# Kernel tuning notes

Hardware: AMD Instinct MI355X
Metric: run time of the kernel (lower is better)

Reference implementation:

```python
import jax, jax.numpy as jnp
import numpy as np

NS = 10000   # servers
ND = 50000   # devices
H = 512      # hidden dim
E = 300000   # edges per relation
L = 4        # total SAGEConv layers (input + 2 hidden + output)


def segment_mean(vals, seg, num_segments):
    # scatter-mean aggregation (PyG 'mean' aggr); empty segments -> 0
    s = jax.ops.segment_sum(vals, seg, num_segments=num_segments)
    cnt = jax.ops.segment_sum(jnp.ones((seg.shape[0], 1), vals.dtype), seg,
                              num_segments=num_segments)
    return s / jnp.maximum(cnt, 1.0)


def setup_inputs() -> dict:
    key = jax.random.key(0)
    ks = jax.random.split(key, 12)
    scale = 0.05
    return {
        "x_servers": jax.random.normal(ks[0], (NS, 64), jnp.float32),
        "x_devices": jax.random.normal(ks[1], (ND, 32), jnp.float32),
        "W_srv": jax.random.normal(ks[2], (64, H), jnp.float32) * scale,
        "b_srv": jnp.zeros((H,), jnp.float32),
        "W_dev": jax.random.normal(ks[3], (32, H), jnp.float32) * scale,
        "b_dev": jnp.zeros((H,), jnp.float32),
        # rel 0: servers->devices (updates devices); rel 1: devices->servers
        "Wl": jax.random.normal(ks[4], (L, 2, H, H), jnp.float32) * scale,
        "bl": jnp.zeros((L, 2, H), jnp.float32),
        "Wr": jax.random.normal(ks[5], (L, 2, H, H), jnp.float32) * scale,
        "e_sd_src": jax.random.randint(ks[6], (E,), 0, NS, jnp.int32),
        "e_sd_dst": jax.random.randint(ks[7], (E,), 0, ND, jnp.int32),
        "e_ds_src": jax.random.randint(ks[8], (E,), 0, ND, jnp.int32),
        "e_ds_dst": jax.random.randint(ks[9], (E,), 0, NS, jnp.int32),
    }


def reference(x_servers, x_devices, W_srv, b_srv, W_dev, b_dev,
              Wl, bl, Wr, e_sd_src, e_sd_dst, e_ds_src, e_ds_dst):
    # per-type input projection (no activation, as in GNN.forward)
    hs = x_servers @ W_srv + b_srv   # [NS, H]
    hd = x_devices @ W_dev + b_dev   # [ND, H]
    for l in range(L):
        # gather source features per edge, scatter-mean to destination
        agg_d = segment_mean(hs[e_sd_src], e_sd_dst, ND)  # servers -> devices
        agg_s = segment_mean(hd[e_ds_src], e_ds_dst, NS)  # devices -> servers
        # SAGEConv: lin_l(agg) + lin_r(x_dst), then relu
        new_d = jax.nn.relu(agg_d @ Wl[l, 0] + bl[l, 0] + hd @ Wr[l, 0])
        new_s = jax.nn.relu(agg_s @ Wl[l, 1] + bl[l, 1] + hs @ Wr[l, 1])
        hs, hd = new_s, new_d
    return (hs, hd)
```

## Files before the change

### kernel.cpp

```cpp
#include <hip/hip_runtime.h>
#include <cstdint>

#define NSRV 10000
#define NDEV 50000
#define HDIM 512
#define NEDGE 300000
#define NLAY 4
#define SCHUNK 2048

typedef unsigned int u32;
typedef unsigned short u16;

typedef __bf16 bf16x8 __attribute__((ext_vector_type(8)));
typedef float f32x4 __attribute__((ext_vector_type(4)));

__device__ __forceinline__ float bflo(u32 u) { return __uint_as_float(u << 16); }
__device__ __forceinline__ float bfhi(u32 u) { return __uint_as_float(u & 0xffff0000u); }
__device__ __forceinline__ float bf2f(u16 v) { return __uint_as_float((u32)v << 16); }
__device__ __forceinline__ u16 f2bf(float f) {
    u32 u = __float_as_uint(f);
    u += 0x7fffu + ((u >> 16) & 1u);
    return (u16)(u >> 16);
}
__device__ __forceinline__ u32 pack2(float a, float b) {
    return (u32)f2bf(a) | ((u32)f2bf(b) << 16);
}

__global__ void cast_bf16(const float* __restrict__ src, u16* __restrict__ dst, int n2) {
    int i = blockIdx.x * 256 + threadIdx.x;
    if (i < n2) {
        float2 v = *(const float2*)(src + 2 * (size_t)i);
        *(u32*)(dst + 2 * (size_t)i) = pack2(v.x, v.y);
    }
}

__global__ void transpose_w(const float* __restrict__ Wl, const float* __restrict__ Wr,
                            u16* __restrict__ WlT, u16* __restrict__ WrT) {
    __shared__ float t[32][33];
    int z = blockIdx.z;
    const float* Wsrc = ((z < 8) ? Wl : Wr) + (size_t)(z & 7) * HDIM * HDIM;
    u16* Wdst = ((z < 8) ? WlT : WrT) + (size_t)(z & 7) * HDIM * HDIM;
    int n0 = blockIdx.x * 32, k0 = blockIdx.y * 32;
    int x = threadIdx.x, y = threadIdx.y;
#pragma unroll
    for (int i = 0; i < 4; ++i)
        t[y + 8 * i][x] = Wsrc[(size_t)(k0 + y + 8 * i) * HDIM + n0 + x];
    __syncthreads();
    if (x < 16) {
#pragma unroll
        for (int i = 0; i < 4; ++i) {
            int n = n0 + y + 8 * i;
            u32 v = pack2(t[2 * x][y + 8 * i], t[2 * x + 1][y + 8 * i]);
            *(u32*)(Wdst + (size_t)n * HDIM + k0 + 2 * x) = v;
        }
    }
}

template <int K>
__global__ void transpose_wp(const float* __restrict__ W, u16* __restrict__ WT) {
    __shared__ float t[32][33];
    int n0 = blockIdx.x * 32, k0 = blockIdx.y * 32;
    int x = threadIdx.x, y = threadIdx.y;
#pragma unroll
    for (int i = 0; i < 4; ++i)
        t[y + 8 * i][x] = W[(size_t)(k0 + y + 8 * i) * HDIM + n0 + x];
    __syncthreads();
    if (x < 16) {
#pragma unroll
        for (int i = 0; i < 4; ++i) {
            int n = n0 + y + 8 * i;
            u32 v = pack2(t[2 * x][y + 8 * i], t[2 * x + 1][y + 8 * i]);
            *(u32*)(WT + (size_t)n * K + k0 + 2 * x) = v;
        }
    }
}

template <int KTOT>
__launch_bounds__(256, 2)
__global__ void proj_gemm(const u16* __restrict__ A, const u16* __restrict__ B,
                          const float* __restrict__ bias, u16* __restrict__ C, int M) {
    constexpr int NKC = KTOT / 8;
    __shared__ __align__(16) u16 As[NKC][128][8];
    __shared__ __align__(16) u16 Bs[NKC][128][8];
    const int tid = threadIdx.x;
    const int lane = tid & 63;
    const int w = tid >> 6;
    const int m0 = blockIdx.x * 128, n0 = blockIdx.y * 128;
    const int wm = w >> 1, wn = w & 1;
    const int g = lane >> 4, r = lane & 15;

    for (int idx = tid; idx < NKC * 128; idx += 256) {
        int row = idx / NKC, kc = idx % NKC;
        int ra = m0 + row; if (ra > M - 1) ra = M - 1;
        *(uint4*)&As[kc][row][0] = *(const uint4*)(A + (size_t)ra * KTOT + kc * 8);
        *(uint4*)&Bs[kc][row][0] = *(const uint4*)(B + (size_t)(n0 + row) * KTOT + kc * 8);
    }
    __syncthreads();

    f32x4 acc[4][4];
#pragma unroll
    for (int i = 0; i < 4; ++i)
#pragma unroll
        for (int j = 0; j < 4; ++j) acc[i][j] = (f32x4){0.f, 0.f, 0.f, 0.f};

#pragma unroll
    for (int t = 0; t < KTOT / 32; ++t) {
        bf16x8 af[4], bfr[4];
#pragma unroll
        for (int i = 0; i < 4; ++i) {
            af[i]  = *(const bf16x8*)&As[t * 4 + g][wm * 64 + i * 16 + r][0];
            bfr[i] = *(const bf16x8*)&Bs[t * 4 + g][wn * 64 + i * 16 + r][0];
        }
#pragma unroll
        for (int i = 0; i < 4; ++i)
#pragma unroll
            for (int j = 0; j < 4; ++j)
                acc[i][j] = __builtin_amdgcn_mfma_f32_16x16x32_bf16(af[i], bfr[j], acc[i][j], 0, 0, 0);
    }
    __syncthreads();

    float bv[4];
#pragma unroll
    for (int j = 0; j < 4; ++j) bv[j] = bias[n0 + wn * 64 + j * 16 + r];

    u16* ep = ((u16*)As) + w * 1024;
    const int rr = lane >> 3;
    const int cc = (lane & 7) * 8;
#pragma unroll
    for (int i = 0; i < 4; ++i) {
#pragma unroll
        for (int j = 0; j < 4; ++j)
#pragma unroll
            for (int q = 0; q < 4; ++q)
                ep[(g * 4 + q) * 64 + j * 16 + r] = f2bf(acc[i][j][q] + bv[j]);
        __syncthreads();
        int row0 = m0 + wm * 64 + i * 16 + rr;
        int row1 = row0 + 8;
        uint4 v0 = *(uint4*)&ep[rr * 64 + cc];
        uint4 v1 = *(uint4*)&ep[(rr + 8) * 64 + cc];
        if (row0 < M) *(uint4*)(C + (size_t)row0 * HDIM + n0 + wn * 64 + cc) = v0;
        if (row1 < M) *(uint4*)(C + (size_t)row1 * HDIM + n0 + wn * 64 + cc) = v1;
        __syncthreads();
    }
}

__global__ void count_k(const int* __restrict__ d_sd, const int* __restrict__ d_ds,
                        int* __restrict__ cd, int* __restrict__ cs) {
    int i = blockIdx.x * 256 + threadIdx.x;
    if (i < NEDGE) atomicAdd(&cd[d_sd[i]], 1);
    else if (i < 2 * NEDGE) atomicAdd(&cs[d_ds[i - NEDGE]], 1);
}

__global__ void scan_a(const int* __restrict__ c, int* __restrict__ o,
                       int* __restrict__ csum, int n) {
    __shared__ int wsum[4];
    int tid = threadIdx.x;
    int base = blockIdx.x * SCHUNK;
    int idx0 = base + tid * 8;
    int v[8];
    int s = 0;
#pragma unroll
    for (int i = 0; i < 8; ++i) {
        int idx = idx0 + i;
        v[i] = (idx < n) ? c[idx] : 0;
        s += v[i];
    }
    int lane = tid & 63, wv = tid >> 6;
    int ss = s;
#pragma unroll
    for (int off = 1; off < 64; off <<= 1) {
        int t = __shfl_up(ss, off);
        if (lane >= off) ss += t;
    }
    if (lane == 63) wsum[wv] = ss;
    __syncthreads();
    int woff = 0;
#pragma unroll
    for (int i = 0; i < 4; ++i)
        if (i < wv) woff += wsum[i];
    int ex = woff + ss - s;
#pragma unroll
    for (int i = 0; i < 8; ++i) {
        int idx = idx0 + i;
        if (idx < n) o[idx] = ex;
        ex += v[i];
    }
    if (tid == 255) csum[blockIdx.x] = woff + ss;
}

__global__ void scan_k(const int* __restrict__ cA, int* __restrict__ oA, int* __restrict__ uA, int nA,
                       const int* __restrict__ cB, int* __restrict__ oB, int* __restrict__ uB, int nB) {
    const int* c; int* o; int* u; int n;
    if (blockIdx.x == 0) { c = cA; o = oA; u = uA; n = nA; }
    else                 { c = cB; o = oB; u = uB; n = nB; }
    int lane = threadIdx.x;
    int carry = 0;
    for (int base = 0; base < n; base += 64) {
        int idx = base + lane;
        int v = (idx < n) ? c[idx] : 0;
        int s = v;
#pragma unroll
        for (int off = 1; off < 64; off <<= 1) {
            int t = __shfl_up(s, off);
            if (lane >= off) s += t;
        }
        if (idx < n) { int ex = carry + s - v; o[idx] = ex; u[idx] = ex; }
        carry += __shfl(s, 63);
    }
}

__global__ void scan_c(int* __restrict__ o, int* __restrict__ cur,
                       const int* __restrict__ csx, int n) {
    int i = blockIdx.x * 256 + threadIdx.x;
    if (i < n) {
        int v = o[i] + csx[i / SCHUNK];
        o[i] = v;
        cur[i] = v;
    }
}

__global__ void fill_k(const int* __restrict__ s_sd, const int* __restrict__ d_sd,
                       int* __restrict__ cur_d, int* __restrict__ srcs_d,
                       const int* __restrict__ s_ds, const int* __restrict__ d_ds,
                       int* __restrict__ cur_s, int* __restrict__ srcs_s) {
    int i = blockIdx.x * 256 + threadIdx.x;
    if (i < NEDGE) {
        int p = atomicAdd(&cur_d[d_sd[i]], 1);
        srcs_d[p] = s_sd[i];
    } else if (i < 2 * NEDGE) {
        int j = i - NEDGE;
        int p = atomicAdd(&cur_s[d_ds[j]], 1);
        srcs_s[p] = s_ds[j];
    }
}

__global__ void aggregate_k(const u16* __restrict__ h, const int* __restrict__ offs,
                            const int* __restrict__ cnt, const int* __restrict__ srcs,
                            u16* __restrict__ agg, int ndst) {
    int wv = threadIdx.x >> 6, lane = threadIdx.x & 63;
    int d = blockIdx.x * 4 + wv;
    if (d >= ndst) return;
    int beg = offs[d], deg = cnt[d];
    float acc[8] = {0.f, 0.f, 0.f, 0.f, 0.f, 0.f, 0.f, 0.f};
    const size_t lanecol = (size_t)lane * 8;
    for (int t0 = 0; t0 < deg; t0 += 64) {
        int nch = min(64, deg - t0);
        int sv = (t0 + lane < deg) ? srcs[beg + t0 + lane] : 0;
        for (int j = 0; j < nch; ++j) {
            int s = __shfl(sv, j);
            const uint4 q = *(const uint4*)(h + (size_t)s * HDIM + lanecol);
            acc[0] += bflo(q.x); acc[1] += bfhi(q.x);
            acc[2] += bflo(q.y); acc[3] += bfhi(q.y);
            acc[4] += bflo(q.z); acc[5] += bfhi(q.z);
            acc[6] += bflo(q.w); acc[7] += bfhi(q.w);
        }
    }
    float sc = 1.f / (float)(deg > 0 ? deg : 1);
    uint4 o;
    o.x = pack2(acc[0] * sc, acc[1] * sc);
    o.y = pack2(acc[2] * sc, acc[3] * sc);
    o.z = pack2(acc[4] * sc, acc[5] * sc);
    o.w = pack2(acc[6] * sc, acc[7] * sc);
    *(uint4*)(agg + (size_t)d * HDIM + lanecol) = o;
}

__launch_bounds__(256, 2)
__global__ void gemm_fused(const u16* __restrict__ A1, const u16* __restrict__ A2,
                           const u16* __restrict__ B1, const u16* __restrict__ B2,
                           const float* __restrict__ bias, u16* __restrict__ C, int M) {
    __shared__ __align__(16) u16 As[2][4][128][8];
    __shared__ __align__(16) u16 Bs[2][4][128][8];
    const int tid = threadIdx.x;
    const int lane = tid & 63;
    const int w = tid >> 6;
    const int m0 = blockIdx.x * 128, n0 = blockIdx.y * 128;
    const int wm = w >> 1, wn = w & 1;
    const int g = lane >> 4, r = lane & 15;

    const int srow = tid >> 2;
    const int skc  = tid & 3;

    f32x4 acc[4][4];
#pragma unroll
    for (int i = 0; i < 4; ++i)
#pragma unroll
        for (int j = 0; j < 4; ++j) acc[i][j] = (f32x4){0.f, 0.f, 0.f, 0.f};

    uint4 ra0, ra1, rb0, rb1;
    auto gload = [&](int kt) {
        const u16* Ap = (kt < 16) ? A1 : A2;
        const u16* Bp = (kt < 16) ? B1 : B2;
        const int kb = (kt & 15) * 32 + skc * 8;
        int r0 = m0 + srow;      if (r0 > M - 1) r0 = M - 1;
        int r1 = m0 + srow + 64; if (r1 > M - 1) r1 = M - 1;
        ra0 = *(const uint4*)(Ap + (size_t)r0 * HDIM + kb);
        ra1 = *(const uint4*)(Ap + (size_t)r1 * HDIM + kb);
        rb0 = *(const uint4*)(Bp + (size_t)(n0 + srow) * HDIM + kb);
        rb1 = *(const uint4*)(Bp + (size_t)(n0 + srow + 64) * HDIM + kb);
    };
    auto swrite = [&](int buf) {
        *(uint4*)&As[buf][skc][srow][0]      = ra0;
        *(uint4*)&As[buf][skc][srow + 64][0] = ra1;
        *(uint4*)&Bs[buf][skc][srow][0]      = rb0;
        *(uint4*)&Bs[buf][skc][srow + 64][0] = rb1;
    };
    auto compute = [&](int buf) {
        bf16x8 af[4], bfr[4];
#pragma unroll
        for (int i = 0; i < 4; ++i) {
            af[i]  = *(const bf16x8*)&As[buf][g][wm * 64 + i * 16 + r][0];
            bfr[i] = *(const bf16x8*)&Bs[buf][g][wn * 64 + i * 16 + r][0];
        }
#pragma unroll
        for (int i = 0; i < 4; ++i)
#pragma unroll
            for (int j = 0; j < 4; ++j)
                acc[i][j] = __builtin_amdgcn_mfma_f32_16x16x32_bf16(af[i], bfr[j], acc[i][j], 0, 0, 0);
    };

    gload(0);
    swrite(0);
    __syncthreads();
    for (int kt = 0; kt < 32; ++kt) {
        if (kt < 31) gload(kt + 1);
        compute(kt & 1);
        if (kt < 31) swrite((kt + 1) & 1);
        __syncthreads();
    }

    float bv[4];
#pragma unroll
    for (int j = 0; j < 4; ++j) bv[j] = bias[n0 + wn * 64 + j * 16 + r];

    u16* ep = ((u16*)As) + w * 1024;
    const int rr = lane >> 3;
    const int cc = (lane & 7) * 8;
#pragma unroll
    for (int i = 0; i < 4; ++i) {
#pragma unroll
        for (int j = 0; j < 4; ++j)
#pragma unroll
            for (int q = 0; q < 4; ++q)
                ep[(g * 4 + q) * 64 + j * 16 + r] = f2bf(fmaxf(acc[i][j][q] + bv[j], 0.f));
        __syncthreads();
        int row0 = m0 + wm * 64 + i * 16 + rr;
        int row1 = row0 + 8;
        uint4 v0 = *(uint4*)&ep[rr * 64 + cc];
        uint4 v1 = *(uint4*)&ep[(rr + 8) * 64 + cc];
        if (row0 < M) *(uint4*)(C + (size_t)row0 * HDIM + n0 + wn * 64 + cc) = v0;
        if (row1 < M) *(uint4*)(C + (size_t)row1 * HDIM + n0 + wn * 64 + cc) = v1;
        __syncthreads();
    }
}

__global__ void expand_k(float* out, int lo, int hi) {
    const u16* src = (const u16*)out;
    int j = lo + blockIdx.x * 256 + threadIdx.x;
    if (j < hi) {
        float v = bf2f(src[j]);
        out[(size_t)j] = v;
    }
}
__global__ void expand_final(float* out, int n) {
    __shared__ u16 tmp[4096];
    const u16* src = (const u16*)out;
    int tid = threadIdx.x;
    for (int i = tid; i < n; i += blockDim.x) tmp[i] = src[i];
    __syncthreads();
    for (int i = tid; i < n; i += blockDim.x) out[(size_t)i] = bf2f(tmp[i]);
}

extern "C" void kernel_launch(void* const* d_in, const int* in_sizes, int n_in,
                              void* d_out, int out_size, void* d_ws, size_t ws_size,
                              hipStream_t stream) {
    const float* x_s   = (const float*)d_in[0];
    const float* x_d   = (const float*)d_in[1];
    const float* W_srv = (const float*)d_in[2];
    const float* b_srv = (const float*)d_in[3];
    const float* W_dev = (const float*)d_in[4];
    const float* b_dev = (const float*)d_in[5];
    const float* Wl    = (const float*)d_in[6];
    const float* bl    = (const float*)d_in[7];
    const float* Wr    = (const float*)d_in[8];
    const int* e_sd_src = (const int*)d_in[9];
    const int* e_sd_dst = (const int*)d_in[10];
    const int* e_ds_src = (const int*)d_in[11];
    const int* e_ds_dst = (const int*)d_in[12];

    const size_t NTOT = (size_t)(NSRV + NDEV) * HDIM;
    float* fout = (float*)d_out;
    u16* u = (u16*)d_out;
    u16* hA_s = u;
    u16* hA_d = u + (size_t)NSRV * HDIM;
    u16* hB_s = u + NTOT;
    u16* hB_d = u + NTOT + (size_t)NSRV * HDIM;

    char* p = (char*)d_ws;
    auto carve = [&](size_t bytes) -> void* {
        void* ret = (void*)p;
        p += (bytes + 255) & ~(size_t)255;
        return ret;
    };
    int* cnt_d = (int*)carve((size_t)NDEV * 4);
    int* cnt_s = (int*)carve((size_t)NSRV * 4);
    int* off_d = (int*)carve((size_t)NDEV * 4);
    int* off_s = (int*)carve((size_t)NSRV * 4);
    int* cur_d = (int*)carve((size_t)NDEV * 4);
    int* cur_s = (int*)carve((size_t)NSRV * 4);
    int* src_d = (int*)carve((size_t)NEDGE * 4);
    int* src_s = (int*)carve((size_t)NEDGE * 4);
    int* csum_d = (int*)carve(64 * 4);
    int* csum_s = (int*)carve(64 * 4);
    int* csx_d  = (int*)carve(64 * 4);
    int* csx_s  = (int*)carve(64 * 4);
    u16* WlT   = (u16*)carve((size_t)NLAY * 2 * HDIM * HDIM * 2);
    u16* WrT   = (u16*)carve((size_t)NLAY * 2 * HDIM * HDIM * 2);
    u16* agg   = (u16*)carve((size_t)NDEV * HDIM * 2);
    u16* xb_s  = (u16*)carve((size_t)NSRV * 64 * 2);
    u16* xb_d  = (u16*)carve((size_t)NDEV * 32 * 2);
    u16* WTp_s = (u16*)carve((size_t)HDIM * 64 * 2);
    u16* WTp_d = (u16*)carve((size_t)HDIM * 32 * 2);

    hipMemsetAsync(cnt_d, 0, (size_t)NDEV * 4, stream);
    hipMemsetAsync(cnt_s, 0, (size_t)NSRV * 4, stream);

    cast_bf16<<<(NSRV * 64 / 2 + 255) / 256, 256, 0, stream>>>(x_s, xb_s, NSRV * 64 / 2);
    cast_bf16<<<(NDEV * 32 / 2 + 255) / 256, 256, 0, stream>>>(x_d, xb_d, NDEV * 32 / 2);
    transpose_wp<64><<<dim3(16, 2), dim3(32, 8), 0, stream>>>(W_srv, WTp_s);
    transpose_wp<32><<<dim3(16, 1), dim3(32, 8), 0, stream>>>(W_dev, WTp_d);
    transpose_w<<<dim3(16, 16, 16), dim3(32, 8), 0, stream>>>(Wl, Wr, WlT, WrT);

    proj_gemm<64><<<dim3((NSRV + 127) / 128, 4), 256, 0, stream>>>(xb_s, WTp_s, b_srv, hA_s, NSRV);
    proj_gemm<32><<<dim3((NDEV + 127) / 128, 4), 256, 0, stream>>>(xb_d, WTp_d, b_dev, hA_d, NDEV);

    count_k<<<(2 * NEDGE + 255) / 256, 256, 0, stream>>>(e_sd_dst, e_ds_dst, cnt_d, cnt_s);

    const int NCH_D = (NDEV + SCHUNK - 1) / SCHUNK;
    const int NCH_S = (NSRV + SCHUNK - 1) / SCHUNK;
    scan_a<<<NCH_D, 256, 0, stream>>>(cnt_d, off_d, csum_d, NDEV);
    scan_a<<<NCH_S, 256, 0, stream>>>(cnt_s, off_s, csum_s, NSRV);
    scan_k<<<2, 64, 0, stream>>>(csum_d, csx_d, csx_d, NCH_D, csum_s, csx_s, csx_s, NCH_S);
    scan_c<<<(NDEV + 255) / 256, 256, 0, stream>>>(off_d, cur_d, csx_d, NDEV);
    scan_c<<<(NSRV + 255) / 256, 256, 0, stream>>>(off_s, cur_s, csx_s, NSRV);

    fill_k<<<(2 * NEDGE + 255) / 256, 256, 0, stream>>>(e_sd_src, e_sd_dst, cur_d, src_d,
                                                        e_ds_src, e_ds_dst, cur_s, src_s);

    for (int l = 0; l < NLAY; ++l) {
        const u16* hs_in = (l & 1) ? hB_s : hA_s;
        const u16* hd_in = (l & 1) ? hB_d : hA_d;
        u16* hs_out = (l & 1) ? hA_s : hB_s;
        u16* hd_out = (l & 1) ? hA_d : hB_d;

        const u16* WlT0 = WlT + (size_t)(l * 2 + 0) * HDIM * HDIM;
        const u16* WrT0 = WrT + (size_t)(l * 2 + 0) * HDIM * HDIM;
        const u16* WlT1 = WlT + (size_t)(l * 2 + 1) * HDIM * HDIM;
        const u16* WrT1 = WrT + (size_t)(l * 2 + 1) * HDIM * HDIM;
        const float* bl0 = bl + (size_t)(l * 2 + 0) * HDIM;
        const float* bl1 = bl + (size_t)(l * 2 + 1) * HDIM;

        aggregate_k<<<(NDEV + 3) / 4, 256, 0, stream>>>(hs_in, off_d, cnt_d, src_d, agg, NDEV);
        gemm_fused<<<dim3((NDEV + 127) / 128, 4), 256, 0, stream>>>(agg, hd_in, WlT0, WrT0, bl0, hd_out, NDEV);
        aggregate_k<<<(NSRV + 3) / 4, 256, 0, stream>>>(hd_in, off_s, cnt_s, src_s, agg, NSRV);
        gemm_fused<<<dim3((NSRV + 127) / 128, 4), 256, 0, stream>>>(agg, hs_in, WlT1, WrT1, bl1, hs_out, NSRV);
    }

    int hi = (int)NTOT;
    while (hi > 4000 && (hi % 2 == 0)) {
        int lo = hi / 2;
        int nblk = (hi - lo + 255) / 256;
        expand_k<<<nblk, 256, 0, stream>>>(fout, lo, hi);
        hi = lo;
    }
    expand_final<<<1, 512, 0, stream>>>(fout, hi);
}
```

Before: 1.042 ms.

## Use direct global-to-LDS loads and grouped tile swizzle in fused SAGE GEMM

```diff
diff --git a/kernel.cpp b/kernel.cpp
--- a/kernel.cpp
+++ b/kernel.cpp
@@ -24,6 +24,13 @@
 }
 __device__ __forceinline__ u32 pack2(float a, float b) {
     return (u32)f2bf(a) | ((u32)f2bf(b) << 16);
+}
+
+__device__ __forceinline__ void gload_lds16(const u16* g, u16* l) {
+    __builtin_amdgcn_global_load_lds(
+        (const __attribute__((address_space(1))) u32*)(uintptr_t)g,
+        (__attribute__((address_space(3))) u32*)(uintptr_t)l,
+        16, 0, 0);
 }
 
 __global__ void cast_bf16(const float* __restrict__ src, u16* __restrict__ dst, int n2) {
@@ -264,45 +271,41 @@
     *(uint4*)(agg + (size_t)d * HDIM + lanecol) = o;
 }
 
-__launch_bounds__(256, 2)
+__launch_bounds__(256, 3)
 __global__ void gemm_fused(const u16* __restrict__ A1, const u16* __restrict__ A2,
                            const u16* __restrict__ B1, const u16* __restrict__ B2,
-                           const float* __restrict__ bias, u16* __restrict__ C, int M) {
+                           const float* __restrict__ bias, u16* __restrict__ C,
+                           int M, int MB) {
+    const int b = blockIdx.x;
+    const int mi = (b >> 5) * 8 + (b & 7);
+    const int ni = (b >> 3) & 3;
+    if (mi >= MB) return;
+
     __shared__ __align__(16) u16 As[2][4][128][8];
     __shared__ __align__(16) u16 Bs[2][4][128][8];
     const int tid = threadIdx.x;
     const int lane = tid & 63;
     const int w = tid >> 6;
-    const int m0 = blockIdx.x * 128, n0 = blockIdx.y * 128;
+    const int m0 = mi * 128, n0 = ni * 128;
     const int wm = w >> 1, wn = w & 1;
     const int g = lane >> 4, r = lane & 15;
 
-    const int srow = tid >> 2;
-    const int skc  = tid & 3;
-
     f32x4 acc[4][4];
 #pragma unroll
     for (int i = 0; i < 4; ++i)
 #pragma unroll
         for (int j = 0; j < 4; ++j) acc[i][j] = (f32x4){0.f, 0.f, 0.f, 0.f};
 
-    uint4 ra0, ra1, rb0, rb1;
-    auto gload = [&](int kt) {
+    auto stage = [&](int buf, int kt) {
         const u16* Ap = (kt < 16) ? A1 : A2;
         const u16* Bp = (kt < 16) ? B1 : B2;
-        const int kb = (kt & 15) * 32 + skc * 8;
-        int r0 = m0 + srow;      if (r0 > M - 1) r0 = M - 1;
-        int r1 = m0 + srow + 64; if (r1 > M - 1) r1 = M - 1;
-        ra0 = *(const uint4*)(Ap + (size_t)r0 * HDIM + kb);
-        ra1 = *(const uint4*)(Ap + (size_t)r1 * HDIM + kb);
-        rb0 = *(const uint4*)(Bp + (size_t)(n0 + srow) * HDIM + kb);
-        rb1 = *(const uint4*)(Bp + (size_t)(n0 + srow + 64) * HDIM + kb);
-    };
-    auto swrite = [&](int buf) {
-        *(uint4*)&As[buf][skc][srow][0]      = ra0;
-        *(uint4*)&As[buf][skc][srow + 64][0] = ra1;
-        *(uint4*)&Bs[buf][skc][srow][0]      = rb0;
-        *(uint4*)&Bs[buf][skc][srow + 64][0] = rb1;
+        const int kb = (kt & 15) * 32 + w * 8;
+        int ra0 = m0 + lane;      if (ra0 > M - 1) ra0 = M - 1;
+        int ra1 = m0 + 64 + lane; if (ra1 > M - 1) ra1 = M - 1;
+        gload_lds16(Ap + (size_t)ra0 * HDIM + kb, &As[buf][w][0][0]);
+        gload_lds16(Ap + (size_t)ra1 * HDIM + kb, &As[buf][w][64][0]);
+        gload_lds16(Bp + (size_t)(n0 + lane) * HDIM + kb,      &Bs[buf][w][0][0]);
+        gload_lds16(Bp + (size_t)(n0 + 64 + lane) * HDIM + kb, &Bs[buf][w][64][0]);
     };
     auto compute = [&](int buf) {
         bf16x8 af[4], bfr[4];
@@ -318,13 +321,11 @@
                 acc[i][j] = __builtin_amdgcn_mfma_f32_16x16x32_bf16(af[i], bfr[j], acc[i][j], 0, 0, 0);
     };
 
-    gload(0);
-    swrite(0);
+    stage(0, 0);
     __syncthreads();
     for (int kt = 0; kt < 32; ++kt) {
-        if (kt < 31) gload(kt + 1);
+        if (kt < 31) stage((kt + 1) & 1, kt + 1);
         compute(kt & 1);
-        if (kt < 31) swrite((kt + 1) & 1);
         __syncthreads();
     }
 
@@ -446,6 +447,11 @@
     fill_k<<<(2 * NEDGE + 255) / 256, 256, 0, stream>>>(e_sd_src, e_sd_dst, cur_d, src_d,
                                                         e_ds_src, e_ds_dst, cur_s, src_s);
 
+    const int MB_D = (NDEV + 127) / 128;
+    const int MB_S = (NSRV + 127) / 128;
+    const int GRID_D = ((MB_D + 7) / 8) * 32;
+    const int GRID_S = ((MB_S + 7) / 8) * 32;
+
     for (int l = 0; l < NLAY; ++l) {
         const u16* hs_in = (l & 1) ? hB_s : hA_s;
         const u16* hd_in = (l & 1) ? hB_d : hA_d;
@@ -460,9 +466,9 @@
         const float* bl1 = bl + (size_t)(l * 2 + 1) * HDIM;
 
         aggregate_k<<<(NDEV + 3) / 4, 256, 0, stream>>>(hs_in, off_d, cnt_d, src_d, agg, NDEV);
-        gemm_fused<<<dim3((NDEV + 127) / 128, 4), 256, 0, stream>>>(agg, hd_in, WlT0, WrT0, bl0, hd_out, NDEV);
+        gemm_fused<<<GRID_D, 256, 0, stream>>>(agg, hd_in, WlT0, WrT0, bl0, hd_out, NDEV, MB_D);
         aggregate_k<<<(NSRV + 3) / 4, 256, 0, stream>>>(hd_in, off_s, cnt_s, src_s, agg, NSRV);
-        gemm_fused<<<dim3((NSRV + 127) / 128, 4), 256, 0, stream>>>(agg, hs_in, WlT1, WrT1, bl1, hs_out, NSRV);
+        gemm_fused<<<GRID_S, 256, 0, stream>>>(agg, hs_in, WlT1, WrT1, bl1, hs_out, NSRV, MB_S);
     }
 
     int hi = (int)NTOT;
```

New measurement: 1.134 ms. +8.9%, slower.
